# Kernel tuning notes

Hardware: AMD Instinct MI355X
Metric: run time of the kernel (lower is better)

The kernel has to match this reference:

```python
import jax, jax.numpy as jnp
import numpy as np

DIM = 1024
N_HEADS = 16

def setup_inputs() -> dict:
    key = jax.random.key(0)
    ks = jax.random.split(key, 6)
    s = 1.0 / np.sqrt(DIM)
    return {
        "x": jax.random.normal(ks[0], (2, 2048, DIM), dtype=jnp.float32),
        "Wq": jax.random.normal(ks[1], (DIM, DIM), dtype=jnp.float32) * s,
        "Wk": jax.random.normal(ks[2], (DIM, DIM), dtype=jnp.float32) * s,
        "Wv": jax.random.normal(ks[3], (DIM, DIM), dtype=jnp.float32) * s,
        "Wo": jax.random.normal(ks[4], (DIM, DIM), dtype=jnp.float32) * s,
        "bo": jax.random.normal(ks[5], (DIM,), dtype=jnp.float32) * 0.01,
    }

def reference(x, Wq, Wk, Wv, Wo, bo):
    B, S, D = x.shape
    H = N_HEADS
    hd = D // H
    # linear layers: y = x @ W.T (torch convention)
    def proj(W):
        y = jnp.einsum('bsd,ed->bse', x, W)
        return y.reshape(B, S, H, hd).transpose(0, 2, 1, 3)  # [B,H,S,hd]
    q, k, v = proj(Wq), proj(Wk), proj(Wv)
    attn = jnp.einsum('bhqd,bhkd->bhqk', q, k) / jnp.sqrt(jnp.float32(hd))
    attn = jax.nn.softmax(attn, axis=-1)
    out = jnp.einsum('bhqk,bhkd->bhqd', attn, v)
    out = out.transpose(0, 2, 1, 3).reshape(B, S, D)
    out = jnp.einsum('bsd,ed->bse', out, Wo) + bo
    return out
```

## Files before the change

### kernel.cpp

```cpp
#include <hip/hip_runtime.h>
#include <hip/hip_bf16.h>

#define SEQ 2048
#define DIM 1024
#define NH 16
#define HD 64
#define MTOT 4096

typedef __attribute__((ext_vector_type(8))) short bf16x8;
typedef __attribute__((ext_vector_type(4))) float f32x4;
typedef __attribute__((ext_vector_type(16))) float f32x16;
typedef __attribute__((ext_vector_type(4))) unsigned int u32x4;
typedef __attribute__((ext_vector_type(2))) unsigned int u32x2;

typedef const __attribute__((address_space(1))) void* gptr_t;
typedef __attribute__((address_space(3))) void* sptr_t;

static __device__ __forceinline__ unsigned short f2bf(float f) {
    unsigned int u = __builtin_bit_cast(unsigned int, f);
    return (unsigned short)((u + 0x7FFFu + ((u >> 16) & 1u)) >> 16);
}

#define CVTPK(d, x, y) asm("v_cvt_pk_bf16_f32 %0, %1, %2" : "=v"(d) : "v"(x), "v"(y))
#define PLSWAP(a, b) asm("v_permlane32_swap_b32 %0, %1" : "+v"(a), "+v"(b))

__global__ void cast_kernel(const float* __restrict__ in, unsigned short* __restrict__ out, int n) {
    int i = (blockIdx.x * 256 + threadIdx.x) * 4;
    if (i < n) {
        float4 v = *reinterpret_cast<const float4*>(in + i);
        ushort4 o;
        o.x = f2bf(v.x); o.y = f2bf(v.y); o.z = f2bf(v.z); o.w = f2bf(v.w);
        *reinterpret_cast<ushort4*>(out + i) = o;
    }
}

template<int MODE>
__global__ __launch_bounds__(256) void gemm_nt(
    const unsigned short* __restrict__ A,
    const unsigned short* __restrict__ B0,
    const unsigned short* __restrict__ B1,
    const unsigned short* __restrict__ B2,
    unsigned short* __restrict__ D0,
    unsigned short* __restrict__ D1,
    unsigned short* __restrict__ D2,
    float* __restrict__ Df,
    const float* __restrict__ bias)
{
    constexpr int K = DIM;
    __shared__ __align__(16) unsigned short Asm[128 * 32];
    __shared__ __align__(16) unsigned short Bsm[128 * 32];

    const int tid = threadIdx.x;
    const int wave = tid >> 6, lane = tid & 63;
    const int wm = wave >> 1, wn = wave & 1;
    const int m0 = blockIdx.y * 128, n0 = blockIdx.x * 128;
    const int fr = lane & 15;

    const unsigned short* Bsel = (MODE == 1 || blockIdx.z == 0) ? B0 : (blockIdx.z == 1 ? B1 : B2);

    const int srow = wave * 32 + (lane >> 2);
    const int schunk = (lane & 3) ^ ((lane >> 3) & 3);
    const size_t abase = (size_t)(m0 + srow) * K + (size_t)schunk * 8;
    const size_t bbase = (size_t)(n0 + srow) * K + (size_t)schunk * 8;

    f32x4 acc[4][4] = {};

    for (int k0 = 0; k0 < K; k0 += 32) {
        #pragma unroll
        for (int c = 0; c < 2; ++c) {
            __builtin_amdgcn_global_load_lds(
                (gptr_t)(A + abase + (size_t)c * 16 * K + k0),
                (sptr_t)((char*)Asm + wave * 2048 + c * 1024), 16, 0, 0);
            __builtin_amdgcn_global_load_lds(
                (gptr_t)(Bsel + bbase + (size_t)c * 16 * K + k0),
                (sptr_t)((char*)Bsm + wave * 2048 + c * 1024), 16, 0, 0);
        }
        __syncthreads();

        bf16x8 af[4], bf[4];
        const int ca = ((lane >> 4) ^ ((fr >> 1) & 3)) * 16;
        #pragma unroll
        for (int i = 0; i < 4; ++i) {
            int ra = wm * 64 + i * 16 + fr;
            int rb = wn * 64 + i * 16 + fr;
            af[i] = *(const bf16x8*)((const char*)Asm + ra * 64 + ca);
            bf[i] = *(const bf16x8*)((const char*)Bsm + rb * 64 + ca);
        }
        #pragma unroll
        for (int i = 0; i < 4; ++i)
            #pragma unroll
            for (int j = 0; j < 4; ++j)
                acc[i][j] = __builtin_amdgcn_mfma_f32_16x16x32_bf16(af[i], bf[j], acc[i][j], 0, 0, 0);
        __syncthreads();
    }

    if (MODE == 0) {
        unsigned short* Dst = (blockIdx.z == 0) ? D0 : (blockIdx.z == 1 ? D1 : D2);
        const float scale = (blockIdx.z == 0) ? 0.1803368787f : 1.0f;
        #pragma unroll
        for (int i = 0; i < 4; ++i)
            #pragma unroll
            for (int j = 0; j < 4; ++j)
                #pragma unroll
                for (int r = 0; r < 4; ++r) {
                    int m = m0 + wm * 64 + i * 16 + (lane >> 4) * 4 + r;
                    int n = n0 + wn * 64 + j * 16 + fr;
                    int b = m >> 11, s = m & 2047, h = n >> 6, dh = n & 63;
                    Dst[(((size_t)(b * NH + h)) * SEQ + s) * HD + dh] = f2bf(acc[i][j][r] * scale);
                }
    } else {
        #pragma unroll
        for (int i = 0; i < 4; ++i)
            #pragma unroll
            for (int j = 0; j < 4; ++j)
                #pragma unroll
                for (int r = 0; r < 4; ++r) {
                    int m = m0 + wm * 64 + i * 16 + (lane >> 4) * 4 + r;
                    int n = n0 + wn * 64 + j * 16 + fr;
                    Df[(size_t)m * DIM + n] = acc[i][j][r] + bias[n];
                }
    }
}

__global__ __launch_bounds__(512, 2) void attn_kernel(
    const unsigned short* __restrict__ Q,
    const unsigned short* __restrict__ Kg,
    const unsigned short* __restrict__ Vg,
    unsigned short* __restrict__ O)
{
    __shared__ __align__(16) char smem[2 * 2 * 8448 * 2];
    unsigned short* Ksm = (unsigned short*)smem;
    unsigned short* Vsm = (unsigned short*)(smem + 2 * 2 * 8448);

    const int tid = threadIdx.x;
    const int wave = tid >> 6, lane = tid & 63;
    const int lq = lane & 31, hi = lane >> 5;
    const int half = wave >> 2, wq = wave & 3;

    const int bid = blockIdx.x;
    const int xcd = bid & 7, slot = bid >> 3;
    const int bh = xcd * 4 + (slot & 3);
    const int q0 = (slot >> 2) * 128;

    const unsigned short* Qh = Q + (size_t)bh * SEQ * HD;
    const unsigned short* Kh = Kg + (size_t)bh * SEQ * HD;
    const unsigned short* Vh = Vg + (size_t)bh * SEQ * HD;

    const int qrow = q0 + wq * 32 + lq;
    bf16x8 qf[4];
    #pragma unroll
    for (int dch = 0; dch < 4; ++dch)
        qf[dch] = *(const bf16x8*)(Qh + (size_t)qrow * HD + dch * 16 + hi * 8);

    f32x16 ot0 = {}, ot1 = {};
    float m = -1e30f, l = 0.f;

    const int tidh = tid & 255;
    const int krow_s = tidh >> 3, kch_s = tidh & 7;
    const int kvp_s = tidh >> 4, sub_s = tidh & 1;
    const int dch_s = (tidh >> 1) & 7;

    bf16x8 sk0, sk1, sv0, sv1;
    auto stage_load = [&](int t64) {
        const int base = t64 + half * 64;
        sk0 = *(const bf16x8*)(Kh + (size_t)(base + krow_s) * HD + kch_s * 8);
        sk1 = *(const bf16x8*)(Kh + (size_t)(base + krow_s + 32) * HD + kch_s * 8);
        sv0 = *(const bf16x8*)(Vh + (size_t)(base + 2 * kvp_s + sub_s) * HD + dch_s * 8);
        sv1 = *(const bf16x8*)(Vh + (size_t)(base + 2 * kvp_s + 32 + sub_s) * HD + dch_s * 8);
    };
    auto vwrite = [&](unsigned* vp, u32x4 vw, int kvp) {
        unsigned p0 = (unsigned)__shfl_xor((int)vw[0], 1);
        unsigned p1 = (unsigned)__shfl_xor((int)vw[1], 1);
        unsigned p2 = (unsigned)__shfl_xor((int)vw[2], 1);
        unsigned p3 = (unsigned)__shfl_xor((int)vw[3], 1);
        unsigned ea0 = sub_s ? p2 : vw[0];
        unsigned ea1 = sub_s ? p3 : vw[1];
        unsigned eb0 = sub_s ? vw[2] : p0;
        unsigned eb1 = sub_s ? vw[3] : p1;
        const int dbase = dch_s * 8 + sub_s * 4;
        vp[33 * (dbase + 0) + kvp] = (ea0 & 0xffffu) | (eb0 << 16);
        vp[33 * (dbase + 1) + kvp] = (ea0 >> 16) | (eb0 & 0xffff0000u);
        vp[33 * (dbase + 2) + kvp] = (ea1 & 0xffffu) | (eb1 << 16);
        vp[33 * (dbase + 3) + kvp] = (ea1 >> 16) | (eb1 & 0xffff0000u);
    };
    auto stage_write = [&](int buf) {
        char* kb = (char*)(Ksm + (size_t)(buf * 2 + half) * 4224);
        u32x4 kw0 = __builtin_bit_cast(u32x4, sk0);
        u32x4 kw1 = __builtin_bit_cast(u32x4, sk1);
        unsigned* kp0 = (unsigned*)(kb + 132 * krow_s + 16 * kch_s);
        unsigned* kp1 = (unsigned*)(kb + 132 * (krow_s + 32) + 16 * kch_s);
        kp0[0] = kw0[0]; kp0[1] = kw0[1]; kp0[2] = kw0[2]; kp0[3] = kw0[3];
        kp1[0] = kw1[0]; kp1[1] = kw1[1]; kp1[2] = kw1[2]; kp1[3] = kw1[3];
        unsigned* vp = (unsigned*)(Vsm + (size_t)(buf * 2 + half) * 4224);
        vwrite(vp, __builtin_bit_cast(u32x4, sv0), kvp_s);
        vwrite(vp, __builtin_bit_cast(u32x4, sv1), kvp_s + 16);
    };

    stage_load(0);
    stage_write(0);
    __syncthreads();

    int cur = 0;
    #pragma unroll 1
    for (int t = 0; t < SEQ / 128; ++t) {
        if (t + 1 < SEQ / 128) stage_load((t + 1) * 128);

        const char* Kb = (const char*)(Ksm + (size_t)(cur * 2 + half) * 4224);
        const char* Vb = (const char*)(Vsm + (size_t)(cur * 2 + half) * 4224);

        f32x16 st0 = {}, st1 = {};
        __builtin_amdgcn_s_setprio(1);
        #pragma unroll
        for (int dch = 0; dch < 4; ++dch) {
            const unsigned* a0 = (const unsigned*)(Kb + 132 * lq + 32 * dch + 16 * hi);
            const unsigned* a1 = (const unsigned*)(Kb + 132 * (32 + lq) + 32 * dch + 16 * hi);
            u32x4 f0 = {a0[0], a0[1], a0[2], a0[3]};
            u32x4 f1 = {a1[0], a1[1], a1[2], a1[3]};
            st0 = __builtin_amdgcn_mfma_f32_32x32x16_bf16(__builtin_bit_cast(bf16x8, f0), qf[dch], st0, 0, 0, 0);
            st1 = __builtin_amdgcn_mfma_f32_32x32x16_bf16(__builtin_bit_cast(bf16x8, f1), qf[dch], st1, 0, 0, 0);
        }
        __builtin_amdgcn_s_setprio(0);

        float pm = st0[0];
        #pragma unroll
        for (int r = 1; r < 16; ++r) pm = fmaxf(pm, st0[r]);
        #pragma unroll
        for (int r = 0; r < 16; ++r) pm = fmaxf(pm, st1[r]);
        pm = fmaxf(pm, __shfl_xor(pm, 32));
        if (__any(pm > m + 8.0f)) {
            float mn = fmaxf(m, pm);
            float fc = exp2f(m - mn);
            l *= fc;
            #pragma unroll
            for (int r = 0; r < 16; ++r) { ot0[r] *= fc; ot1[r] *= fc; }
            m = mn;
        }
        float ps = 0.f;
        #pragma unroll
        for (int r = 0; r < 16; ++r) { st0[r] = exp2f(st0[r] - m); ps += st0[r]; }
        #pragma unroll
        for (int r = 0; r < 16; ++r) { st1[r] = exp2f(st1[r] - m); ps += st1[r]; }
        ps += __shfl_xor(ps, 32);
        l += ps;

        bf16x8 pf0, pf1, pf2, pf3;
        {
            unsigned w0, w1, w2, w3, w4, w5, w6, w7;
            CVTPK(w0, st0[0], st0[1]);   CVTPK(w1, st0[2], st0[3]);
            CVTPK(w2, st0[4], st0[5]);   CVTPK(w3, st0[6], st0[7]);
            CVTPK(w4, st0[8], st0[9]);   CVTPK(w5, st0[10], st0[11]);
            CVTPK(w6, st0[12], st0[13]); CVTPK(w7, st0[14], st0[15]);
            PLSWAP(w0, w2); PLSWAP(w1, w3); PLSWAP(w4, w6); PLSWAP(w5, w7);
            u32x4 uA = {w0, w1, w2, w3}, uB = {w4, w5, w6, w7};
            pf0 = __builtin_bit_cast(bf16x8, uA);
            pf1 = __builtin_bit_cast(bf16x8, uB);
        }
        {
            unsigned w0, w1, w2, w3, w4, w5, w6, w7;
            CVTPK(w0, st1[0], st1[1]);   CVTPK(w1, st1[2], st1[3]);
            CVTPK(w2, st1[4], st1[5]);   CVTPK(w3, st1[6], st1[7]);
            CVTPK(w4, st1[8], st1[9]);   CVTPK(w5, st1[10], st1[11]);
            CVTPK(w6, st1[12], st1[13]); CVTPK(w7, st1[14], st1[15]);
            PLSWAP(w0, w2); PLSWAP(w1, w3); PLSWAP(w4, w6); PLSWAP(w5, w7);
            u32x4 uA = {w0, w1, w2, w3}, uB = {w4, w5, w6, w7};
            pf2 = __builtin_bit_cast(bf16x8, uA);
            pf3 = __builtin_bit_cast(bf16x8, uB);
        }

        __builtin_amdgcn_s_setprio(1);
        #pragma unroll
        for (int kc = 0; kc < 4; ++kc) {
            const unsigned* v0 = (const unsigned*)(Vb + 132 * lq + 32 * kc + 16 * hi);
            const unsigned* v1 = (const unsigned*)(Vb + 132 * (32 + lq) + 32 * kc + 16 * hi);
            u32x4 g0 = {v0[0], v0[1], v0[2], v0[3]};
            u32x4 g1 = {v1[0], v1[1], v1[2], v1[3]};
            bf16x8 pfv = (kc == 0) ? pf0 : (kc == 1) ? pf1 : (kc == 2) ? pf2 : pf3;
            ot0 = __builtin_amdgcn_mfma_f32_32x32x16_bf16(__builtin_bit_cast(bf16x8, g0), pfv, ot0, 0, 0, 0);
            ot1 = __builtin_amdgcn_mfma_f32_32x32x16_bf16(__builtin_bit_cast(bf16x8, g1), pfv, ot1, 0, 0, 0);
        }
        __builtin_amdgcn_s_setprio(0);

        if (t + 1 < SEQ / 128) stage_write(cur ^ 1);
        __syncthreads();
        cur ^= 1;
    }

    __syncthreads();
    float* mg = (float*)smem;
    const int mbase = (wq * 64 + lane) * 34;
    if (half == 1) {
        mg[mbase + 0] = m;
        mg[mbase + 1] = l;
        #pragma unroll
        for (int r = 0; r < 16; ++r) { mg[mbase + 2 + r] = ot0[r]; mg[mbase + 18 + r] = ot1[r]; }
    }
    __syncthreads();
    if (half == 0) {
        float m2 = mg[mbase + 0], l2 = mg[mbase + 1];
        float mn = fmaxf(m, m2);
        float f1 = exp2f(m - mn), f2 = exp2f(m2 - mn);
        float inv = 1.0f / (l * f1 + l2 * f2);
        f1 *= inv; f2 *= inv;

        const int b = bh >> 4, h = bh & 15;
        unsigned short* orow = O + ((size_t)(b * SEQ + qrow)) * DIM + h * HD;
        #pragma unroll
        for (int tg = 0; tg < 4; ++tg) {
            unsigned wA, wB;
            float a0 = ot0[4 * tg + 0] * f1 + mg[mbase + 2 + 4 * tg + 0] * f2;
            float a1 = ot0[4 * tg + 1] * f1 + mg[mbase + 2 + 4 * tg + 1] * f2;
            float a2 = ot0[4 * tg + 2] * f1 + mg[mbase + 2 + 4 * tg + 2] * f2;
            float a3 = ot0[4 * tg + 3] * f1 + mg[mbase + 2 + 4 * tg + 3] * f2;
            CVTPK(wA, a0, a1); CVTPK(wB, a2, a3);
            u32x2 wlo = {wA, wB};
            *(u32x2*)(orow + 8 * tg + 4 * hi) = wlo;
            float b0 = ot1[4 * tg + 0] * f1 + mg[mbase + 18 + 4 * tg + 0] * f2;
            float b1 = ot1[4 * tg + 1] * f1 + mg[mbase + 18 + 4 * tg + 1] * f2;
            float b2 = ot1[4 * tg + 2] * f1 + mg[mbase + 18 + 4 * tg + 2] * f2;
            float b3 = ot1[4 * tg + 3] * f1 + mg[mbase + 18 + 4 * tg + 3] * f2;
            CVTPK(wA, b0, b1); CVTPK(wB, b2, b3);
            u32x2 whi = {wA, wB};
            *(u32x2*)(orow + 32 + 8 * tg + 4 * hi) = whi;
        }
    }
}

extern "C" void kernel_launch(void* const* d_in, const int* in_sizes, int n_in,
                              void* d_out, int out_size, void* d_ws, size_t ws_size,
                              hipStream_t stream) {
    const float* x  = (const float*)d_in[0];
    const float* Wq = (const float*)d_in[1];
    const float* Wk = (const float*)d_in[2];
    const float* Wv = (const float*)d_in[3];
    const float* Wo = (const float*)d_in[4];
    const float* bo = (const float*)d_in[5];
    float* out = (float*)d_out;

    unsigned short* ws = (unsigned short*)d_ws;
    unsigned short* xb  = ws;
    unsigned short* wqb = xb + (size_t)MTOT * DIM;
    unsigned short* wkb = wqb + (size_t)DIM * DIM;
    unsigned short* wvb = wkb + (size_t)DIM * DIM;
    unsigned short* wob = wvb + (size_t)DIM * DIM;
    unsigned short* qb  = wob + (size_t)DIM * DIM;
    unsigned short* kb  = qb + (size_t)MTOT * DIM;
    unsigned short* vb  = kb + (size_t)MTOT * DIM;
    unsigned short* ob  = vb + (size_t)MTOT * DIM;

    cast_kernel<<<dim3(MTOT * DIM / 1024), 256, 0, stream>>>(x, xb, MTOT * DIM);
    cast_kernel<<<dim3(DIM * DIM / 1024), 256, 0, stream>>>(Wq, wqb, DIM * DIM);
    cast_kernel<<<dim3(DIM * DIM / 1024), 256, 0, stream>>>(Wk, wkb, DIM * DIM);
    cast_kernel<<<dim3(DIM * DIM / 1024), 256, 0, stream>>>(Wv, wvb, DIM * DIM);
    cast_kernel<<<dim3(DIM * DIM / 1024), 256, 0, stream>>>(Wo, wob, DIM * DIM);

    gemm_nt<0><<<dim3(DIM / 128, MTOT / 128, 3), 256, 0, stream>>>(
        xb, wqb, wkb, wvb, qb, kb, vb, nullptr, nullptr);

    attn_kernel<<<dim3(512), 512, 0, stream>>>(qb, kb, vb, ob);

    gemm_nt<1><<<dim3(DIM / 128, MTOT / 128, 1), 256, 0, stream>>>(
        ob, wob, nullptr, nullptr, nullptr, nullptr, nullptr, out, bo);
}
```

Before: 147.5 us.

## Write V transposed from projection GEMM and load K/V fragments directly from global

The QKV projection epilogue now writes V in a head-major transposed layout [b,h,dh,s] with packed bf16 stores. The attention kernel drops the LDS double-buffered K/V staging and its __syncthreads, and instead loads MFMA operand fragments for K and V straight from global memory, relying on L2 reuse across waves. Launch bounds are raised to allow more resident blocks, and the max and sum reductions are split into four independent chains. This removes LDS traffic and barriers, but each wave now loads K/V redundantly from global memory with no explicit prefetch ahead of use.

Result: slower. 219.3 us (+48.7%).

```diff
diff --git a/kernel.cpp b/kernel.cpp
--- a/kernel.cpp
+++ b/kernel.cpp
@@ -95,19 +95,36 @@
     }
 
     if (MODE == 0) {
-        unsigned short* Dst = (blockIdx.z == 0) ? D0 : (blockIdx.z == 1 ? D1 : D2);
-        const float scale = (blockIdx.z == 0) ? 0.1803368787f : 1.0f;
-        #pragma unroll
-        for (int i = 0; i < 4; ++i)
-            #pragma unroll
-            for (int j = 0; j < 4; ++j)
+        if (blockIdx.z == 2) {
+            #pragma unroll
+            for (int i = 0; i < 4; ++i)
                 #pragma unroll
-                for (int r = 0; r < 4; ++r) {
-                    int m = m0 + wm * 64 + i * 16 + (lane >> 4) * 4 + r;
+                for (int j = 0; j < 4; ++j) {
                     int n = n0 + wn * 64 + j * 16 + fr;
-                    int b = m >> 11, s = m & 2047, h = n >> 6, dh = n & 63;
-                    Dst[(((size_t)(b * NH + h)) * SEQ + s) * HD + dh] = f2bf(acc[i][j][r] * scale);
+                    int h = n >> 6, dh = n & 63;
+                    int mb = m0 + wm * 64 + i * 16 + (lane >> 4) * 4;
+                    int b = mb >> 11, s = mb & 2047;
+                    unsigned wA, wB;
+                    CVTPK(wA, acc[i][j][0], acc[i][j][1]);
+                    CVTPK(wB, acc[i][j][2], acc[i][j][3]);
+                    u32x2 w = {wA, wB};
+                    *(u32x2*)(D2 + ((size_t)((b * NH + h) * HD + dh)) * SEQ + s) = w;
                 }
+        } else {
+            unsigned short* Dst = (blockIdx.z == 0) ? D0 : D1;
+            const float scale = (blockIdx.z == 0) ? 0.1803368787f : 1.0f;
+            #pragma unroll
+            for (int i = 0; i < 4; ++i)
+                #pragma unroll
+                for (int j = 0; j < 4; ++j)
+                    #pragma unroll
+                    for (int r = 0; r < 4; ++r) {
+                        int m = m0 + wm * 64 + i * 16 + (lane >> 4) * 4 + r;
+                        int n = n0 + wn * 64 + j * 16 + fr;
+                        int b = m >> 11, s = m & 2047, h = n >> 6, dh = n & 63;
+                        Dst[(((size_t)(b * NH + h)) * SEQ + s) * HD + dh] = f2bf(acc[i][j][r] * scale);
+                    }
+        }
     } else {
         #pragma unroll
         for (int i = 0; i < 4; ++i)
@@ -122,15 +139,13 @@
     }
 }
 
-__global__ __launch_bounds__(512, 2) void attn_kernel(
+__global__ __launch_bounds__(512, 4) void attn_kernel(
     const unsigned short* __restrict__ Q,
     const unsigned short* __restrict__ Kg,
-    const unsigned short* __restrict__ Vg,
+    const unsigned short* __restrict__ Vt,
     unsigned short* __restrict__ O)
 {
-    __shared__ __align__(16) char smem[2 * 2 * 8448 * 2];
-    unsigned short* Ksm = (unsigned short*)smem;
-    unsigned short* Vsm = (unsigned short*)(smem + 2 * 2 * 8448);
+    __shared__ float mg[4 * 64 * 34];
 
     const int tid = threadIdx.x;
     const int wave = tid >> 6, lane = tid & 63;
@@ -144,7 +159,7 @@
 
     const unsigned short* Qh = Q + (size_t)bh * SEQ * HD;
     const unsigned short* Kh = Kg + (size_t)bh * SEQ * HD;
-    const unsigned short* Vh = Vg + (size_t)bh * SEQ * HD;
+    const unsigned short* Vh = Vt + (size_t)bh * HD * SEQ;
 
     const int qrow = q0 + wq * 32 + lq;
     bf16x8 qf[4];
@@ -155,77 +170,48 @@
     f32x16 ot0 = {}, ot1 = {};
     float m = -1e30f, l = 0.f;
 
-    const int tidh = tid & 255;
-    const int krow_s = tidh >> 3, kch_s = tidh & 7;
-    const int kvp_s = tidh >> 4, sub_s = tidh & 1;
-    const int dch_s = (tidh >> 1) & 7;
-
-    bf16x8 sk0, sk1, sv0, sv1;
-    auto stage_load = [&](int t64) {
-        const int base = t64 + half * 64;
-        sk0 = *(const bf16x8*)(Kh + (size_t)(base + krow_s) * HD + kch_s * 8);
-        sk1 = *(const bf16x8*)(Kh + (size_t)(base + krow_s + 32) * HD + kch_s * 8);
-        sv0 = *(const bf16x8*)(Vh + (size_t)(base + 2 * kvp_s + sub_s) * HD + dch_s * 8);
-        sv1 = *(const bf16x8*)(Vh + (size_t)(base + 2 * kvp_s + 32 + sub_s) * HD + dch_s * 8);
-    };
-    auto vwrite = [&](unsigned* vp, u32x4 vw, int kvp) {
-        unsigned p0 = (unsigned)__shfl_xor((int)vw[0], 1);
-        unsigned p1 = (unsigned)__shfl_xor((int)vw[1], 1);
-        unsigned p2 = (unsigned)__shfl_xor((int)vw[2], 1);
-        unsigned p3 = (unsigned)__shfl_xor((int)vw[3], 1);
-        unsigned ea0 = sub_s ? p2 : vw[0];
-        unsigned ea1 = sub_s ? p3 : vw[1];
-        unsigned eb0 = sub_s ? vw[2] : p0;
-        unsigned eb1 = sub_s ? vw[3] : p1;
-        const int dbase = dch_s * 8 + sub_s * 4;
-        vp[33 * (dbase + 0) + kvp] = (ea0 & 0xffffu) | (eb0 << 16);
-        vp[33 * (dbase + 1) + kvp] = (ea0 >> 16) | (eb0 & 0xffff0000u);
-        vp[33 * (dbase + 2) + kvp] = (ea1 & 0xffffu) | (eb1 << 16);
-        vp[33 * (dbase + 3) + kvp] = (ea1 >> 16) | (eb1 & 0xffff0000u);
-    };
-    auto stage_write = [&](int buf) {
-        char* kb = (char*)(Ksm + (size_t)(buf * 2 + half) * 4224);
-        u32x4 kw0 = __builtin_bit_cast(u32x4, sk0);
-        u32x4 kw1 = __builtin_bit_cast(u32x4, sk1);
-        unsigned* kp0 = (unsigned*)(kb + 132 * krow_s + 16 * kch_s);
-        unsigned* kp1 = (unsigned*)(kb + 132 * (krow_s + 32) + 16 * kch_s);
-        kp0[0] = kw0[0]; kp0[1] = kw0[1]; kp0[2] = kw0[2]; kp0[3] = kw0[3];
-        kp1[0] = kw1[0]; kp1[1] = kw1[1]; kp1[2] = kw1[2]; kp1[3] = kw1[3];
-        unsigned* vp = (unsigned*)(Vsm + (size_t)(buf * 2 + half) * 4224);
-        vwrite(vp, __builtin_bit_cast(u32x4, sv0), kvp_s);
-        vwrite(vp, __builtin_bit_cast(u32x4, sv1), kvp_s + 16);
-    };
-
-    stage_load(0);
-    stage_write(0);
-    __syncthreads();
-
-    int cur = 0;
+    const unsigned short* Kp = Kh + (size_t)lq * HD + hi * 8;
+    const unsigned short* Vp = Vh + (size_t)lq * SEQ + hi * 8;
+
     #pragma unroll 1
-    for (int t = 0; t < SEQ / 128; ++t) {
-        if (t + 1 < SEQ / 128) stage_load((t + 1) * 128);
-
-        const char* Kb = (const char*)(Ksm + (size_t)(cur * 2 + half) * 4224);
-        const char* Vb = (const char*)(Vsm + (size_t)(cur * 2 + half) * 4224);
+    for (int tt = 0; tt < SEQ / 128; ++tt) {
+        const int kvb = half * 64 + tt * 128;
+
+        bf16x8 kf0[4], kf1[4];
+        #pragma unroll
+        for (int dch = 0; dch < 4; ++dch) {
+            kf0[dch] = *(const bf16x8*)(Kp + (size_t)kvb * HD + dch * 16);
+            kf1[dch] = *(const bf16x8*)(Kp + (size_t)(kvb + 32) * HD + dch * 16);
+        }
 
         f32x16 st0 = {}, st1 = {};
         __builtin_amdgcn_s_setprio(1);
         #pragma unroll
         for (int dch = 0; dch < 4; ++dch) {
-            const unsigned* a0 = (const unsigned*)(Kb + 132 * lq + 32 * dch + 16 * hi);
-            const unsigned* a1 = (const unsigned*)(Kb + 132 * (32 + lq) + 32 * dch + 16 * hi);
-            u32x4 f0 = {a0[0], a0[1], a0[2], a0[3]};
-            u32x4 f1 = {a1[0], a1[1], a1[2], a1[3]};
-            st0 = __builtin_amdgcn_mfma_f32_32x32x16_bf16(__builtin_bit_cast(bf16x8, f0), qf[dch], st0, 0, 0, 0);
-            st1 = __builtin_amdgcn_mfma_f32_32x32x16_bf16(__builtin_bit_cast(bf16x8, f1), qf[dch], st1, 0, 0, 0);
+            st0 = __builtin_amdgcn_mfma_f32_32x32x16_bf16(kf0[dch], qf[dch], st0, 0, 0, 0);
+            st1 = __builtin_amdgcn_mfma_f32_32x32x16_bf16(kf1[dch], qf[dch], st1, 0, 0, 0);
         }
         __builtin_amdgcn_s_setprio(0);
 
-        float pm = st0[0];
-        #pragma unroll
-        for (int r = 1; r < 16; ++r) pm = fmaxf(pm, st0[r]);
-        #pragma unroll
-        for (int r = 0; r < 16; ++r) pm = fmaxf(pm, st1[r]);
+        bf16x8 vf0[4], vf1[4];
+        #pragma unroll
+        for (int kc = 0; kc < 4; ++kc) {
+            vf0[kc] = *(const bf16x8*)(Vp + kvb + kc * 16);
+            vf1[kc] = *(const bf16x8*)(Vp + (size_t)32 * SEQ + kvb + kc * 16);
+        }
+
+        float pa = st0[0], pb = st0[1], pc = st0[2], pd = st0[3];
+        #pragma unroll
+        for (int r = 4; r < 16; r += 4) {
+            pa = fmaxf(pa, st0[r]); pb = fmaxf(pb, st0[r + 1]);
+            pc = fmaxf(pc, st0[r + 2]); pd = fmaxf(pd, st0[r + 3]);
+        }
+        #pragma unroll
+        for (int r = 0; r < 16; r += 4) {
+            pa = fmaxf(pa, st1[r]); pb = fmaxf(pb, st1[r + 1]);
+            pc = fmaxf(pc, st1[r + 2]); pd = fmaxf(pd, st1[r + 3]);
+        }
+        float pm = fmaxf(fmaxf(pa, pb), fmaxf(pc, pd));
         pm = fmaxf(pm, __shfl_xor(pm, 32));
         if (__any(pm > m + 8.0f)) {
             float mn = fmaxf(m, pm);
@@ -235,11 +221,22 @@
             for (int r = 0; r < 16; ++r) { ot0[r] *= fc; ot1[r] *= fc; }
             m = mn;
         }
-        float ps = 0.f;
-        #pragma unroll
-        for (int r = 0; r < 16; ++r) { st0[r] = exp2f(st0[r] - m); ps += st0[r]; }
-        #pragma unroll
-        for (int r = 0; r < 16; ++r) { st1[r] = exp2f(st1[r] - m); ps += st1[r]; }
+        float sa = 0.f, sb = 0.f, sc = 0.f, sd = 0.f;
+        #pragma unroll
+        for (int r = 0; r < 16; r += 4) {
+            st0[r] = exp2f(st0[r] - m);     sa += st0[r];
+            st0[r + 1] = exp2f(st0[r + 1] - m); sb += st0[r + 1];
+            st0[r + 2] = exp2f(st0[r + 2] - m); sc += st0[r + 2];
+            st0[r + 3] = exp2f(st0[r + 3] - m); sd += st0[r + 3];
+        }
+        #pragma unroll
+        for (int r = 0; r < 16; r += 4) {
+            st1[r] = exp2f(st1[r] - m);     sa += st1[r];
+            st1[r + 1] = exp2f(st1[r + 1] - m); sb += st1[r + 1];
+            st1[r + 2] = exp2f(st1[r + 2] - m); sc += st1[r + 2];
+            st1[r + 3] = exp2f(st1[r + 3] - m); sd += st1[r + 3];
+        }
+        float ps = (sa + sb) + (sc + sd);
         ps += __shfl_xor(ps, 32);
         l += ps;
 
@@ -270,23 +267,13 @@
         __builtin_amdgcn_s_setprio(1);
         #pragma unroll
         for (int kc = 0; kc < 4; ++kc) {
-            const unsigned* v0 = (const unsigned*)(Vb + 132 * lq + 32 * kc + 16 * hi);
-            const unsigned* v1 = (const unsigned*)(Vb + 132 * (32 + lq) + 32 * kc + 16 * hi);
-            u32x4 g0 = {v0[0], v0[1], v0[2], v0[3]};
-            u32x4 g1 = {v1[0], v1[1], v1[2], v1[3]};
             bf16x8 pfv = (kc == 0) ? pf0 : (kc == 1) ? pf1 : (kc == 2) ? pf2 : pf3;
-            ot0 = __builtin_amdgcn_mfma_f32_32x32x16_bf16(__builtin_bit_cast(bf16x8, g0), pfv, ot0, 0, 0, 0);
-            ot1 = __builtin_amdgcn_mfma_f32_32x32x16_bf16(__builtin_bit_cast(bf16x8, g1), pfv, ot1, 0, 0, 0);
+            ot0 = __builtin_amdgcn_mfma_f32_32x32x16_bf16(vf0[kc], pfv, ot0, 0, 0, 0);
+            ot1 = __builtin_amdgcn_mfma_f32_32x32x16_bf16(vf1[kc], pfv, ot1, 0, 0, 0);
         }
         __builtin_amdgcn_s_setprio(0);
-
-        if (t + 1 < SEQ / 128) stage_write(cur ^ 1);
-        __syncthreads();
-        cur ^= 1;
-    }
-
-    __syncthreads();
-    float* mg = (float*)smem;
+    }
+
     const int mbase = (wq * 64 + lane) * 34;
     if (half == 1) {
         mg[mbase + 0] = m;
@@ -344,8 +331,8 @@
     unsigned short* wob = wvb + (size_t)DIM * DIM;
     unsigned short* qb  = wob + (size_t)DIM * DIM;
     unsigned short* kb  = qb + (size_t)MTOT * DIM;
-    unsigned short* vb  = kb + (size_t)MTOT * DIM;
-    unsigned short* ob  = vb + (size_t)MTOT * DIM;
+    unsigned short* vtb = kb + (size_t)MTOT * DIM;
+    unsigned short* ob  = vtb + (size_t)MTOT * DIM;
 
     cast_kernel<<<dim3(MTOT * DIM / 1024), 256, 0, stream>>>(x, xb, MTOT * DIM);
     cast_kernel<<<dim3(DIM * DIM / 1024), 256, 0, stream>>>(Wq, wqb, DIM * DIM);
@@ -354,9 +341,9 @@
     cast_kernel<<<dim3(DIM * DIM / 1024), 256, 0, stream>>>(Wo, wob, DIM * DIM);
 
     gemm_nt<0><<<dim3(DIM / 128, MTOT / 128, 3), 256, 0, stream>>>(
-        xb, wqb, wkb, wvb, qb, kb, vb, nullptr, nullptr);
-
-    attn_kernel<<<dim3(512), 512, 0, stream>>>(qb, kb, vb, ob);
+        xb, wqb, wkb, wvb, qb, kb, vtb, nullptr, nullptr);
+
+    attn_kernel<<<dim3(512), 512, 0, stream>>>(qb, kb, vtb, ob);
 
     gemm_nt<1><<<dim3(DIM / 128, MTOT / 128, 1), 256, 0, stream>>>(
         ob, wob, nullptr, nullptr, nullptr, nullptr, nullptr, out, bo);
```
